# Kernel optimization log

Measured on AMD Instinct MI355X. Metric: run time of the kernel, lower is better.

## Reference

```python
import jax, jax.numpy as jnp
import numpy as np

DEPTH, DIM, HEADS, MLP_HID, POS_DIM, PROJ_DIM, NCLS, INP = 5, 128, 8, 256, 128, 128, 1000, 35
EPS = 1e-5

def _ln(x, g, b):
    m = x.mean(-1, keepdims=True)
    v = ((x - m) ** 2).mean(-1, keepdims=True)
    return (x - m) / jnp.sqrt(v + EPS) * g + b

def _gelu(x):
    return jax.nn.gelu(x, approximate=False)  # torch nn.GELU default (erf)

def setup_inputs() -> dict:
    key = jax.random.key(0)
    ks = iter(jax.random.split(key, 80))
    nxt = lambda: next(ks)
    B, N = 8, 1024
    w = lambda *s: (jax.random.normal(nxt(), s, jnp.float32) / np.sqrt(s[-2]).astype(np.float32))
    z = lambda *s: jnp.zeros(s, jnp.float32)
    o = lambda *s: jnp.ones(s, jnp.float32)
    node_feat = jax.random.normal(nxt(), (B, N, 3), jnp.float32)
    a = (jax.random.uniform(nxt(), (B, N, N)) < 0.01).astype(jnp.float32)
    adj = jnp.maximum(a, a.transpose(0, 2, 1))  # symmetric 0/1 adjacency
    lapl = jax.random.normal(nxt(), (B, N, 32), jnp.float32) * 0.1
    d = dict(
        node_feat=node_feat, adj=adj, lapl=lapl,
        cls_token=jax.random.normal(nxt(), (1, 1, DIM), jnp.float32),
        pe_w1=w(INP, 2 * INP), pe_b1=z(2 * INP),
        pe_w2=w(2 * INP, 2 * INP), pe_b2=z(2 * INP),
        pe_w3=w(2 * INP, 2 * INP), pe_b3=z(2 * INP),
        pe_lng=o(2 * INP), pe_lnb=z(2 * INP),
        pe_w4=w(2 * INP, POS_DIM), pe_b4=z(POS_DIM),
        blk_ln1_g=o(DEPTH, DIM), blk_ln1_b=z(DEPTH, DIM),
        blk_qkv_w=w(DEPTH, DIM, 3 * HEADS * DIM),
        blk_proj_w=w(DEPTH, HEADS * DIM, DIM), blk_proj_b=z(DEPTH, DIM),
        blk_gamma_w=jax.random.uniform(nxt(), (DEPTH, DIM, 2), jnp.float32) * 0.01,
        blk_gamma_b=z(DEPTH, 2),
        blk_ln2_g=o(DEPTH, DIM), blk_ln2_b=z(DEPTH, DIM),
        blk_mlp_w1=w(DEPTH, DIM, MLP_HID), blk_mlp_b1=z(DEPTH, MLP_HID),
        blk_mlp_w2=w(DEPTH, MLP_HID, DIM), blk_mlp_b2=z(DEPTH, DIM),
        head_lng=o(DIM), head_lnb=z(DIM), head_w=w(DIM, DIM), head_b=z(DIM),
        proj_w1=w(DIM, PROJ_DIM), proj_b1=z(PROJ_DIM),
        proj_w2=w(PROJ_DIM, PROJ_DIM), proj_b2=z(PROJ_DIM),
        proj_w3=w(PROJ_DIM, PROJ_DIM), proj_b3=z(PROJ_DIM),
        proj_lng=o(PROJ_DIM), proj_lnb=z(PROJ_DIM),
        proj_w4=w(PROJ_DIM, NCLS), proj_b4=z(NCLS),
    )
    return d

def reference(node_feat, adj, lapl, cls_token, pe_w1, pe_b1, pe_w2, pe_b2, pe_w3, pe_b3,
              pe_lng, pe_lnb, pe_w4, pe_b4, blk_ln1_g, blk_ln1_b, blk_qkv_w, blk_proj_w,
              blk_proj_b, blk_gamma_w, blk_gamma_b, blk_ln2_g, blk_ln2_b, blk_mlp_w1,
              blk_mlp_b1, blk_mlp_w2, blk_mlp_b2, head_lng, head_lnb, head_w, head_b,
              proj_w1, proj_b1, proj_w2, proj_b2, proj_w3, proj_b3, proj_lng, proj_lnb,
              proj_w4, proj_b4):
    B, N, _ = node_feat.shape
    M = N + 1
    # positional-encoding MLP on concatenated [node_feat | lapl] (inp_dim = 35)
    x = jnp.concatenate([node_feat, lapl], axis=2)
    x = _gelu(x @ pe_w1 + pe_b1)
    x = _gelu(x @ pe_w2 + pe_b2)
    x = _gelu(x @ pe_w3 + pe_b3)
    x = _ln(x, pe_lng, pe_lnb) @ pe_w4 + pe_b4  # [B,N,DIM]
    x = jnp.concatenate([jnp.broadcast_to(cls_token, (B, 1, DIM)), x], axis=1)  # [B,M,DIM]
    # adjacency with cls row/col, adj_cls[:,0,0] = 1
    adj_cls = jnp.zeros((B, M, M), x.dtype).at[:, 0, 0].set(1.0).at[:, 1:, 1:].set(adj)
    scale = DIM ** (-0.5)
    for i in range(DEPTH):
        h = _ln(x, blk_ln1_g[i], blk_ln1_b[i])
        qkv = (h @ blk_qkv_w[i]).reshape(B, M, 3, HEADS, DIM).transpose(2, 0, 3, 1, 4)
        q, k, v = qkv[0], qkv[1], qkv[2]  # each [B,H,M,D]
        attn = jnp.einsum('bhnd,bhmd->bhnm', q, k) * scale
        gamma = jnp.exp(h @ blk_gamma_w[i] + blk_gamma_b[i])  # [B,M,2], use_exp=True
        attn = gamma[:, None, :, 0:1] * attn + gamma[:, None, :, 1:2] * adj_cls[:, None]
        attn = jax.nn.softmax(attn, axis=-1)
        o = jnp.einsum('bhnm,bhmd->bhnd', attn, v).transpose(0, 2, 1, 3).reshape(B, M, HEADS * DIM)
        x = o @ blk_proj_w[i] + blk_proj_b[i] + h  # residual from normed input (as in source)
        h2 = _ln(x, blk_ln2_g[i], blk_ln2_b[i])
        x = _gelu(h2 @ blk_mlp_w1[i] + blk_mlp_b1[i]) @ blk_mlp_w2[i] + blk_mlp_b2[i] + h2
    c = x[:, 0]
    c = _ln(c, head_lng, head_lnb) @ head_w + head_b  # mlp_head
    p = _gelu(c @ proj_w1 + proj_b1)
    p = _gelu(p @ proj_w2 + proj_b2)
    p = _gelu(p @ proj_w3 + proj_b3)
    p = _ln(p, proj_lng, proj_lnb) @ proj_w4 + proj_b4
    return (c, p)
```

## Files before the change

### kernel.cpp

```cpp
#include <hip/hip_runtime.h>
#include <hip/hip_bf16.h>
#include <math.h>

#define NB 8
#define NSEQ 1024
#define M_ 1025
#define ROWS (NB * M_)
#define DIMC 128
#define NHEADS 8
#define QKV3 3072
#define PEROWS (NB * NSEQ)
#define ACS 1088

typedef __attribute__((ext_vector_type(8))) short bf16x8;
typedef __attribute__((ext_vector_type(4))) float f32x4;

__device__ __forceinline__ float gelu_f(float x) {
  return 0.5f * x * (1.f + erff(x * 0.70710678118654752440f));
}

__device__ __forceinline__ unsigned short f2bf(float f) {
  __hip_bfloat16 h = __float2bfloat16(f);
  return *reinterpret_cast<unsigned short*>(&h);
}

__device__ __forceinline__ float bf2f(unsigned short u) {
  union { unsigned int i; float f; } c;
  c.i = ((unsigned int)u) << 16;
  return c.f;
}

__device__ __forceinline__ void g2lds16(const void* g, void* l) {
  __builtin_amdgcn_global_load_lds(
      (__attribute__((address_space(1))) void*)(g),
      (__attribute__((address_space(3))) void*)(l), 16, 0, 0);
}

template<int K, int KP, int C, int SS, int DOGELU>
__device__ __forceinline__ void pe_stage(
    int tid, const float* __restrict__ W, const float* __restrict__ B,
    const float* src, float* dst, float (*wb)[128])
{
  for (int i = tid; i < K * C; i += 128) wb[i / C][i % C] = W[i];
  if (tid < C) {
#pragma unroll
    for (int k = K; k < KP; ++k) wb[k][tid] = 0.f;
  }
  __syncthreads();
  if (tid < C) {
    float acc[16];
#pragma unroll
    for (int r = 0; r < 16; ++r) acc[r] = B[tid];
#pragma unroll 1
    for (int k4 = 0; k4 < KP; k4 += 4) {
      const float w0 = wb[k4 + 0][tid];
      const float w1 = wb[k4 + 1][tid];
      const float w2 = wb[k4 + 2][tid];
      const float w3 = wb[k4 + 3][tid];
#pragma unroll
      for (int r = 0; r < 16; ++r) {
        const float4 av = *(const float4*)&src[r * SS + k4];
        acc[r] = fmaf(av.x, w0, acc[r]);
        acc[r] = fmaf(av.y, w1, acc[r]);
        acc[r] = fmaf(av.z, w2, acc[r]);
        acc[r] = fmaf(av.w, w3, acc[r]);
      }
    }
#pragma unroll
    for (int r = 0; r < 16; ++r) dst[r * 72 + tid] = DOGELU ? gelu_f(acc[r]) : acc[r];
  }
  __syncthreads();
}

__global__ __launch_bounds__(128) void pe_fused_k(
    const float* __restrict__ nf, const float* __restrict__ lp,
    const float* __restrict__ w1, const float* __restrict__ b1,
    const float* __restrict__ w2, const float* __restrict__ b2,
    const float* __restrict__ w3, const float* __restrict__ b3,
    const float* __restrict__ lng, const float* __restrict__ lnb,
    const float* __restrict__ w4, const float* __restrict__ b4,
    float* __restrict__ x)
{
  __shared__ float sIn[16][36];
  __shared__ float sX[16][72];
  __shared__ float sY[16][72];
  __shared__ float wb[72][128];
  const int tid = threadIdx.x;
  const int r0 = blockIdx.x * 16;

  for (int i = tid; i < 16 * 35; i += 128) {
    const int r = i / 35, c = i - r * 35;
    const int gr = r0 + r;
    sIn[r][c] = (c < 3) ? nf[(size_t)gr * 3 + c] : lp[(size_t)gr * 32 + (c - 3)];
  }
  if (tid < 16) {
    sIn[tid][35] = 0.f;
    sX[tid][70] = 0.f; sX[tid][71] = 0.f;
    sY[tid][70] = 0.f; sY[tid][71] = 0.f;
  }
  __syncthreads();

  pe_stage<35, 36, 70, 36, 1>(tid, w1, b1, &sIn[0][0], &sX[0][0], wb);
  pe_stage<70, 72, 70, 72, 1>(tid, w2, b2, &sX[0][0], &sY[0][0], wb);
  pe_stage<70, 72, 70, 72, 1>(tid, w3, b3, &sY[0][0], &sX[0][0], wb);

  if (tid < 16) {
    float m = 0.f;
    for (int d = 0; d < 70; ++d) m += sX[tid][d];
    m *= (1.f / 70.f);
    float v = 0.f;
    for (int d = 0; d < 70; ++d) { const float t = sX[tid][d] - m; v += t * t; }
    const float inv = rsqrtf(v * (1.f / 70.f) + 1e-5f);
    for (int d = 0; d < 70; ++d) sX[tid][d] = (sX[tid][d] - m) * inv * lng[d] + lnb[d];
  }
  __syncthreads();

  {
    for (int i = tid; i < 70 * 128; i += 128) wb[i >> 7][i & 127] = w4[i];
#pragma unroll
    for (int k = 70; k < 72; ++k) wb[k][tid] = 0.f;
    __syncthreads();
    float acc[16];
#pragma unroll
    for (int r = 0; r < 16; ++r) acc[r] = b4[tid];
#pragma unroll 1
    for (int k4 = 0; k4 < 72; k4 += 4) {
      const float w0 = wb[k4 + 0][tid];
      const float w1v = wb[k4 + 1][tid];
      const float w2v = wb[k4 + 2][tid];
      const float w3v = wb[k4 + 3][tid];
#pragma unroll
      for (int r = 0; r < 16; ++r) {
        const float4 av = *(const float4*)&sX[r][k4];
        acc[r] = fmaf(av.x, w0, acc[r]);
        acc[r] = fmaf(av.y, w1v, acc[r]);
        acc[r] = fmaf(av.z, w2v, acc[r]);
        acc[r] = fmaf(av.w, w3v, acc[r]);
      }
    }
#pragma unroll
    for (int r = 0; r < 16; ++r) {
      const int gr = r0 + r;
      x[(size_t)(gr + gr / 1024 + 1) * DIMC + tid] = acc[r];
    }
  }
}

template<int ACT, int OBF, int RES>
__global__ __launch_bounds__(256) void mgemm_k(
    const unsigned short* __restrict__ Xb, const unsigned short* __restrict__ Wt,
    const float* __restrict__ bias, const float* __restrict__ res,
    void* __restrict__ outp, int rows, int K, int N)
{
  __shared__ unsigned short sX[64][72];
  __shared__ unsigned short sW[64][72];
  const int tid = threadIdx.x;
  const int w = tid >> 6, lane = tid & 63;
  const int col = lane & 15, quad = lane >> 4;
  const int r0 = blockIdx.x * 64, n0 = blockIdx.y * 64;
  const int lr = tid >> 2, lc = tid & 3;
  const int xrow = min(r0 + lr, rows - 1);
  const unsigned short* xsrc = Xb + (size_t)xrow * K + lc * 8;
  const unsigned short* wsrc = Wt + (size_t)(n0 + lr) * K + lc * 8;

  f32x4 acc[4];
#pragma unroll
  for (int t = 0; t < 4; ++t) acc[t] = (f32x4){0.f, 0.f, 0.f, 0.f};

  for (int k0 = 0; k0 < K; k0 += 64) {
    __syncthreads();
    *(uint4*)&sX[lr][lc * 8]      = *(const uint4*)(xsrc + k0);
    *(uint4*)&sX[lr][lc * 8 + 32] = *(const uint4*)(xsrc + k0 + 32);
    *(uint4*)&sW[lr][lc * 8]      = *(const uint4*)(wsrc + k0);
    *(uint4*)&sW[lr][lc * 8 + 32] = *(const uint4*)(wsrc + k0 + 32);
    __syncthreads();
    const bf16x8 aX0 = *(const bf16x8*)&sX[w * 16 + col][quad * 8];
    const bf16x8 aX1 = *(const bf16x8*)&sX[w * 16 + col][32 + quad * 8];
#pragma unroll
    for (int t = 0; t < 4; ++t) {
      const bf16x8 bW0 = *(const bf16x8*)&sW[t * 16 + col][quad * 8];
      const bf16x8 bW1 = *(const bf16x8*)&sW[t * 16 + col][32 + quad * 8];
      acc[t] = __builtin_amdgcn_mfma_f32_16x16x32_bf16(aX0, bW0, acc[t], 0, 0, 0);
      acc[t] = __builtin_amdgcn_mfma_f32_16x16x32_bf16(aX1, bW1, acc[t], 0, 0, 0);
    }
  }
  const int gr_base = r0 + w * 16 + quad * 4;
#pragma unroll
  for (int t = 0; t < 4; ++t) {
    const int n = n0 + t * 16 + col;
    const float bv = bias ? bias[n] : 0.f;
#pragma unroll
    for (int r = 0; r < 4; ++r) {
      const int gr = gr_base + r;
      if (gr < rows) {
        float v = acc[t][r] + bv;
        if (ACT) v = gelu_f(v);
        if (RES) v += res[(size_t)gr * N + n];
        if (OBF) ((unsigned short*)outp)[(size_t)gr * N + n] = f2bf(v);
        else     ((float*)outp)[(size_t)gr * N + n] = v;
      }
    }
  }
}

template<int DOLN, int GAMMA, int WRITEX>
__global__ __launch_bounds__(256) void mgemm_ln_k(
    const unsigned short* __restrict__ Xb, const unsigned short* __restrict__ Wt,
    const float* __restrict__ bias, const float* __restrict__ res,
    const float* __restrict__ lng, const float* __restrict__ lnb,
    const float* __restrict__ gw, const float* __restrict__ gb,
    float* __restrict__ xout, float* __restrict__ h,
    unsigned short* __restrict__ hb, float* __restrict__ gamout,
    int rows, int K)
{
  __shared__ unsigned short sX[64][72];
  __shared__ unsigned short sW[128][72];
  const int tid = threadIdx.x;
  const int w = tid >> 6, lane = tid & 63;
  const int col = lane & 15, quad = lane >> 4;
  const int r0 = blockIdx.x * 64;

  f32x4 acc[8];
#pragma unroll
  for (int t = 0; t < 8; ++t) acc[t] = (f32x4){0.f, 0.f, 0.f, 0.f};

  for (int k0 = 0; k0 < K; k0 += 64) {
    __syncthreads();
#pragma unroll
    for (int l = 0; l < 2; ++l) {
      const int idx = l * 256 + tid;
      const int row = idx >> 3, c = idx & 7;
      const int xrow = min(r0 + row, rows - 1);
      *(uint4*)&sX[row][c * 8] = *(const uint4*)(Xb + (size_t)xrow * K + k0 + c * 8);
    }
#pragma unroll
    for (int l = 0; l < 4; ++l) {
      const int idx = l * 256 + tid;
      const int row = idx >> 3, c = idx & 7;
      *(uint4*)&sW[row][c * 8] = *(const uint4*)(Wt + (size_t)row * K + k0 + c * 8);
    }
    __syncthreads();
    const bf16x8 aX0 = *(const bf16x8*)&sX[w * 16 + col][quad * 8];
    const bf16x8 aX1 = *(const bf16x8*)&sX[w * 16 + col][32 + quad * 8];
#pragma unroll
    for (int t = 0; t < 8; ++t) {
      const bf16x8 bW0 = *(const bf16x8*)&sW[t * 16 + col][quad * 8];
      const bf16x8 bW1 = *(const bf16x8*)&sW[t * 16 + col][32 + quad * 8];
      acc[t] = __builtin_amdgcn_mfma_f32_16x16x32_bf16(aX0, bW0, acc[t], 0, 0, 0);
      acc[t] = __builtin_amdgcn_mfma_f32_16x16x32_bf16(aX1, bW1, acc[t], 0, 0, 0);
    }
  }

  const int gr_base = r0 + w * 16 + quad * 4;
  float bv[8];
#pragma unroll
  for (int t = 0; t < 8; ++t) bv[t] = bias[t * 16 + col];
  float val[8][4];
#pragma unroll
  for (int r = 0; r < 4; ++r) {
    const int grc = min(gr_base + r, rows - 1);
#pragma unroll
    for (int t = 0; t < 8; ++t)
      val[t][r] = acc[t][r] + bv[t] + res[(size_t)grc * DIMC + t * 16 + col];
  }
  if (WRITEX) {
#pragma unroll
    for (int r = 0; r < 4; ++r) {
      const int gr = gr_base + r;
      if (gr < rows) {
#pragma unroll
        for (int t = 0; t < 8; ++t)
          xout[(size_t)gr * DIMC + t * 16 + col] = val[t][r];
      }
    }
  }
  if (DOLN) {
    float lg[8], lb[8], gwa[8], gwb[8];
#pragma unroll
    for (int t = 0; t < 8; ++t) {
      lg[t] = lng[t * 16 + col];
      lb[t] = lnb[t * 16 + col];
      if (GAMMA) { gwa[t] = gw[2 * (t * 16 + col)]; gwb[t] = gw[2 * (t * 16 + col) + 1]; }
    }
#pragma unroll
    for (int r = 0; r < 4; ++r) {
      const int gr = gr_base + r;
      float s = 0.f;
#pragma unroll
      for (int t = 0; t < 8; ++t) s += val[t][r];
      s += __shfl_xor(s, 1); s += __shfl_xor(s, 2);
      s += __shfl_xor(s, 4); s += __shfl_xor(s, 8);
      const float mean = s * (1.f / 128.f);
      float vv = 0.f;
#pragma unroll
      for (int t = 0; t < 8; ++t) { const float d = val[t][r] - mean; vv += d * d; }
      vv += __shfl_xor(vv, 1); vv += __shfl_xor(vv, 2);
      vv += __shfl_xor(vv, 4); vv += __shfl_xor(vv, 8);
      const float inv = rsqrtf(vv * (1.f / 128.f) + 1e-5f);
      float a0 = 0.f, a1 = 0.f;
#pragma unroll
      for (int t = 0; t < 8; ++t) {
        const float o = (val[t][r] - mean) * inv * lg[t] + lb[t];
        if (gr < rows) {
          h[(size_t)gr * DIMC + t * 16 + col] = o;
          hb[(size_t)gr * DIMC + t * 16 + col] = f2bf(o);
        }
        if (GAMMA) { a0 = fmaf(o, gwa[t], a0); a1 = fmaf(o, gwb[t], a1); }
      }
      if (GAMMA) {
        a0 += __shfl_xor(a0, 1); a0 += __shfl_xor(a0, 2);
        a0 += __shfl_xor(a0, 4); a0 += __shfl_xor(a0, 8);
        a1 += __shfl_xor(a1, 1); a1 += __shfl_xor(a1, 2);
        a1 += __shfl_xor(a1, 4); a1 += __shfl_xor(a1, 8);
        if (col == 0 && gr < rows) {
          gamout[(size_t)gr * 2 + 0] = expf(a0 + gb[0]);
          gamout[(size_t)gr * 2 + 1] = expf(a1 + gb[1]);
        }
      }
    }
  }
}

template<int OBF, int VT>
__global__ __launch_bounds__(256) void mgemm128_k(
    const unsigned short* __restrict__ Xb, const unsigned short* __restrict__ Wt,
    const float* __restrict__ bias, void* __restrict__ outp,
    unsigned short* __restrict__ vtp, int rows, int K, int N)
{
  __shared__ unsigned short sX[128][72];
  __shared__ unsigned short sW[128][72];
  const int tid = threadIdx.x;
  const int w = tid >> 6, lane = tid & 63;
  const int col = lane & 15, quad = lane >> 4;
  const int wr = w >> 1, wc = w & 1;
  const int r0 = blockIdx.x * 128, n0 = blockIdx.y * 128;

  f32x4 acc[4][4];
#pragma unroll
  for (int i = 0; i < 4; ++i)
#pragma unroll
    for (int j = 0; j < 4; ++j) acc[i][j] = (f32x4){0.f, 0.f, 0.f, 0.f};

  for (int k0 = 0; k0 < K; k0 += 64) {
    __syncthreads();
#pragma unroll
    for (int l = 0; l < 4; ++l) {
      const int idx = l * 256 + tid;
      const int row = idx >> 3, c = idx & 7;
      const int xrow = min(r0 + row, rows - 1);
      *(uint4*)&sX[row][c * 8] = *(const uint4*)(Xb + (size_t)xrow * K + k0 + c * 8);
      *(uint4*)&sW[row][c * 8] = *(const uint4*)(Wt + (size_t)(n0 + row) * K + k0 + c * 8);
    }
    __syncthreads();
    bf16x8 aX[4][2];
#pragma unroll
    for (int i = 0; i < 4; ++i) {
      aX[i][0] = *(const bf16x8*)&sX[wr * 64 + i * 16 + col][quad * 8];
      aX[i][1] = *(const bf16x8*)&sX[wr * 64 + i * 16 + col][32 + quad * 8];
    }
#pragma unroll
    for (int j = 0; j < 4; ++j) {
      const bf16x8 b0 = *(const bf16x8*)&sW[wc * 64 + j * 16 + col][quad * 8];
      const bf16x8 b1 = *(const bf16x8*)&sW[wc * 64 + j * 16 + col][32 + quad * 8];
#pragma unroll
      for (int i = 0; i < 4; ++i) {
        acc[i][j] = __builtin_amdgcn_mfma_f32_16x16x32_bf16(aX[i][0], b0, acc[i][j], 0, 0, 0);
        acc[i][j] = __builtin_amdgcn_mfma_f32_16x16x32_bf16(aX[i][1], b1, acc[i][j], 0, 0, 0);
      }
    }
  }
  const bool dovt = VT && (n0 >= 2048);
#pragma unroll
  for (int i = 0; i < 4; ++i) {
    const int gr_base = r0 + wr * 64 + i * 16 + quad * 4;
    int bb[4], mm[4];
    if (dovt) {
#pragma unroll
      for (int r = 0; r < 4; ++r) {
        const int gr = gr_base + r;
        bb[r] = gr / 1025;
        mm[r] = gr - bb[r] * 1025;
      }
    }
#pragma unroll
    for (int j = 0; j < 4; ++j) {
      const int n = n0 + wc * 64 + j * 16 + col;
      const float bv = bias ? bias[n] : 0.f;
      const int hh = (n - 2048) >> 7;
      const int d  = (n - 2048) & 127;
#pragma unroll
      for (int r = 0; r < 4; ++r) {
        const int gr = gr_base + r;
        if (gr < rows) {
          const float v = acc[i][j][r] + bv;
          const unsigned short bf = f2bf(v);
          if (OBF) ((unsigned short*)outp)[(size_t)gr * N + n] = bf;
          else     ((float*)outp)[(size_t)gr * N + n] = v;
          if (dovt) vtp[(((size_t)(bb[r] * NHEADS + hh) * DIMC + d) * ACS) + mm[r]] = bf;
        }
      }
    }
  }
}

__global__ __launch_bounds__(256) void ln_rows_k(
    const float* __restrict__ in, float* __restrict__ out,
    unsigned short* __restrict__ outb,
    const float* __restrict__ g, const float* __restrict__ b,
    const float* __restrict__ gw, const float* __restrict__ gb,
    float* __restrict__ gamout, int rows, int D)
{
  const int wv = (blockIdx.x * blockDim.x + threadIdx.x) >> 6;
  const int lane = threadIdx.x & 63;
  if (wv >= rows) return;
  const float* r = in + (size_t)wv * D;
  float s = 0.f;
  for (int d = lane; d < D; d += 64) s += r[d];
  for (int off = 32; off; off >>= 1) s += __shfl_down(s, off);
  const float mean = __shfl(s, 0) / (float)D;
  float v = 0.f;
  for (int d = lane; d < D; d += 64) { float t = r[d] - mean; v += t * t; }
  for (int off = 32; off; off >>= 1) v += __shfl_down(v, off);
  const float inv = rsqrtf(__shfl(v, 0) / (float)D + 1e-5f);
  float* orow = out + (size_t)wv * D;
  float a0 = 0.f, a1 = 0.f;
  for (int d = lane; d < D; d += 64) {
    const float o = (r[d] - mean) * inv * g[d] + b[d];
    orow[d] = o;
    if (outb) outb[(size_t)wv * D + d] = f2bf(o);
    if (gw) { a0 = fmaf(o, gw[2 * d], a0); a1 = fmaf(o, gw[2 * d + 1], a1); }
  }
  if (gw) {
    for (int off = 32; off; off >>= 1) { a0 += __shfl_down(a0, off); a1 += __shfl_down(a1, off); }
    if (lane == 0) {
      gamout[(size_t)wv * 2 + 0] = expf(a0 + gb[0]);
      gamout[(size_t)wv * 2 + 1] = expf(a1 + gb[1]);
    }
  }
}

__global__ __launch_bounds__(256) void adjp_k(const float* __restrict__ adj,
                                              unsigned long long* __restrict__ adjp)
{
  const int n = blockIdx.x;
  const int b = blockIdx.y;
  const int wv = threadIdx.x >> 6, lane = threadIdx.x & 63;
  for (int w = wv; w < 17; w += 4) {
    const int m = w * 64 + lane;
    float av = 0.f;
    if (n == 0) av = (m == 0) ? 1.f : 0.f;
    else if (m >= 1 && m <= NSEQ) av = adj[((size_t)b * NSEQ + (n - 1)) * NSEQ + (m - 1)];
    const unsigned long long mask = __ballot(av != 0.f);
    if (lane == 0) adjp[((size_t)b * M_ + n) * 17 + w] = mask;
  }
}

__global__ void wtrans_k(const float* __restrict__ W, unsigned short* __restrict__ Wt,
                         int K, int N)
{
  __shared__ float t[32][33];
  const int k0 = blockIdx.x * 32, n0 = blockIdx.y * 32;
  const float* Wd = W + (size_t)blockIdx.z * K * N;
  unsigned short* Wtd = Wt + (size_t)blockIdx.z * K * N;
  for (int i = threadIdx.y; i < 32; i += 8)
    t[i][threadIdx.x] = Wd[(size_t)(k0 + i) * N + n0 + threadIdx.x];
  __syncthreads();
  for (int i = threadIdx.y; i < 32; i += 8)
    Wtd[(size_t)(n0 + i) * K + k0 + threadIdx.x] = f2bf(t[threadIdx.x][i]);
}

__global__ __launch_bounds__(512) void attn_mfma_k(
    const unsigned short* __restrict__ qkv, const float* __restrict__ gamma,
    const unsigned long long* __restrict__ adjp, const unsigned short* __restrict__ vt,
    unsigned short* __restrict__ o)
{
  __shared__ unsigned short sK[2][64][128];
  __shared__ unsigned short sVt[2][128][64];
  __shared__ unsigned short sP[256][64];

  const int hh = blockIdx.x, qt = blockIdx.y, b = blockIdx.z;
  const int tid = threadIdx.x;
  const int w = tid >> 6;
  const int lane = tid & 63;
  const int col = lane & 15;
  const int quad = lane >> 4;
  const int qbase = qt * 256 + w * 32;
  const float scale = 0.088388347648318447f;

  bf16x8 aQ[2][4];
#pragma unroll
  for (int rg = 0; rg < 2; ++rg) {
    const int qrow = qbase + rg * 16 + col;
    const unsigned short* qp = qkv + ((size_t)(b * M_ + qrow)) * QKV3 + hh * DIMC + quad * 8;
#pragma unroll
    for (int c = 0; c < 4; ++c) aQ[rg][c] = *(const bf16x8*)(qp + c * 32);
  }
  float g0[2][4], g1[2][4];
  int adjo[2][4];
#pragma unroll
  for (int rg = 0; rg < 2; ++rg)
#pragma unroll
    for (int r = 0; r < 4; ++r) {
      const int nc = qbase + rg * 16 + quad * 4 + r;
      g0[rg][r] = gamma[(size_t)(b * M_ + nc) * 2 + 0] * scale;
      g1[rg][r] = gamma[(size_t)(b * M_ + nc) * 2 + 1];
      adjo[rg][r] = (b * M_ + nc) * 17;
    }

  float l_i[2][4] = {{0.f, 0.f, 0.f, 0.f}, {0.f, 0.f, 0.f, 0.f}};
  f32x4 Oacc[2][8];
#pragma unroll
  for (int rg = 0; rg < 2; ++rg)
#pragma unroll
    for (int t = 0; t < 8; ++t) Oacc[rg][t] = (f32x4){0.f, 0.f, 0.f, 0.f};

  const size_t vtbase = ((size_t)(b * NHEADS + hh)) * DIMC * ACS;

  auto stageK = [&](int buf, int kt_) {
#pragma unroll
    for (int l = 0; l < 2; ++l) {
      const int m = l * 32 + w * 4 + (lane >> 4);
      const int gm = min(kt_ * 64 + m, 1024);
      const unsigned short* src = qkv + ((size_t)(b * M_ + gm)) * QKV3 + 1024
                                  + hh * DIMC + (((lane & 15) ^ (m & 7)) * 8);
      g2lds16(src, &sK[buf][l * 32 + w * 4][0]);
    }
  };
  auto stageV = [&](int buf, int kt_) {
#pragma unroll
    for (int l = 0; l < 2; ++l) {
      const int d = l * 64 + w * 8 + (lane >> 3);
      const unsigned short* src = vt + vtbase + (size_t)d * ACS + kt_ * 64
                                  + (((lane & 7) ^ (d & 7)) * 8);
      g2lds16(src, &sVt[buf][l * 64 + w * 8][0]);
    }
  };

  stageK(0, 0);
  stageV(0, 0);

  int cur = 0;
  for (int kt = 0; kt < 17; ++kt) {
    const int m0 = kt * 64;
    asm volatile("s_waitcnt vmcnt(0)" ::: "memory");
    __builtin_amdgcn_s_barrier();
    __builtin_amdgcn_sched_barrier(0);

    const bool more = (kt < 16);
    if (more) {
      stageK(cur ^ 1, kt + 1);
      stageV(cur ^ 1, kt + 1);
    }

    unsigned long long mk[2][4];
#pragma unroll
    for (int rg = 0; rg < 2; ++rg)
#pragma unroll
      for (int r = 0; r < 4; ++r) mk[rg][r] = adjp[adjo[rg][r] + kt];

    f32x4 Sacc[2][4];
#pragma unroll
    for (int rg = 0; rg < 2; ++rg)
#pragma unroll
      for (int t = 0; t < 4; ++t) Sacc[rg][t] = (f32x4){0.f, 0.f, 0.f, 0.f};
    __builtin_amdgcn_s_setprio(1);
#pragma unroll
    for (int t = 0; t < 4; ++t) {
#pragma unroll
      for (int c = 0; c < 4; ++c) {
        const bf16x8 bK = *(const bf16x8*)&sK[cur][t * 16 + col][((c * 4 + quad) ^ (col & 7)) * 8];
        Sacc[0][t] = __builtin_amdgcn_mfma_f32_16x16x32_bf16(aQ[0][c], bK, Sacc[0][t], 0, 0, 0);
        Sacc[1][t] = __builtin_amdgcn_mfma_f32_16x16x32_bf16(aQ[1][c], bK, Sacc[1][t], 0, 0, 0);
      }
    }
    __builtin_amdgcn_s_setprio(0);

#pragma unroll
    for (int t = 0; t < 4; ++t) {
      const int m = m0 + t * 16 + col;
      const bool mv = (m < M_);
      const int chb = t * 2 + (col >> 3);
      const int sh = t * 16 + col;
#pragma unroll
      for (int rg = 0; rg < 2; ++rg)
#pragma unroll
        for (int r = 0; r < 4; ++r) {
          const float bias = ((mk[rg][r] >> sh) & 1ull) ? g1[rg][r] : 0.f;
          const float s = fmaf(g0[rg][r], Sacc[rg][t][r], bias);
          const float pv = mv ? __expf(s) : 0.f;
          l_i[rg][r] += pv;
          const int ql = w * 32 + rg * 16 + quad * 4 + r;
          sP[ql][((chb ^ (ql & 7)) * 8) + (col & 7)] = f2bf(pv);
        }
    }

    __builtin_amdgcn_s_setprio(1);
#pragma unroll
    for (int ch = 0; ch < 2; ++ch) {
      const int pr = w * 32 + col;
      const bf16x8 aP0 = *(const bf16x8*)&sP[pr][((ch * 4 + quad) ^ (col & 7)) * 8];
      const bf16x8 aP1 = *(const bf16x8*)&sP[pr + 16][((ch * 4 + quad) ^ (col & 7)) * 8];
#pragma unroll
      for (int t = 0; t < 8; ++t) {
        const bf16x8 bV = *(const bf16x8*)&sVt[cur][t * 16 + col][((ch * 4 + quad) ^ (col & 7)) * 8];
        Oacc[0][t] = __builtin_amdgcn_mfma_f32_16x16x32_bf16(aP0, bV, Oacc[0][t], 0, 0, 0);
        Oacc[1][t] = __builtin_amdgcn_mfma_f32_16x16x32_bf16(aP1, bV, Oacc[1][t], 0, 0, 0);
      }
    }
    __builtin_amdgcn_s_setprio(0);
    cur ^= 1;
  }

#pragma unroll
  for (int rg = 0; rg < 2; ++rg)
#pragma unroll
    for (int r = 0; r < 4; ++r) {
      float s = l_i[rg][r];
      s += __shfl_xor(s, 1);
      s += __shfl_xor(s, 2);
      s += __shfl_xor(s, 4);
      s += __shfl_xor(s, 8);
      const int n = qbase + rg * 16 + quad * 4 + r;
      const float invl = 1.f / s;
      unsigned short* orow = o + ((size_t)(b * M_ + n)) * (NHEADS * DIMC) + hh * DIMC + col;
#pragma unroll
      for (int t = 0; t < 8; ++t) orow[t * 16] = f2bf(Oacc[rg][t][r] * invl);
    }
}

__global__ __launch_bounds__(256) void cls_attn_k(
    const unsigned short* __restrict__ qkv, const float* __restrict__ gamma,
    const unsigned long long* __restrict__ adjp, const unsigned short* __restrict__ vt,
    unsigned short* __restrict__ o)
{
  __shared__ float qf[DIMC];
  __shared__ float pbuf[1056];
  __shared__ float lred[4];
  __shared__ float oshare[DIMC];
  const int hh = blockIdx.x & 7, b = blockIdx.x >> 3;
  const int tid = threadIdx.x;
  const size_t rowbase = (size_t)b * M_ + 1024;

  if (tid < DIMC) qf[tid] = bf2f(qkv[rowbase * QKV3 + hh * DIMC + tid]);
  __syncthreads();
  const float g0 = gamma[rowbase * 2 + 0] * 0.088388347648318447f;
  const float g1 = gamma[rowbase * 2 + 1];

  float lpart = 0.f;
  for (int m = tid; m < M_; m += 256) {
    const unsigned short* kp = qkv + ((size_t)(b * M_ + m)) * QKV3 + 1024 + hh * DIMC;
    float s = 0.f;
#pragma unroll
    for (int d0 = 0; d0 < DIMC; d0 += 8) {
      const bf16x8 kv = *(const bf16x8*)(kp + d0);
#pragma unroll
      for (int j = 0; j < 8; ++j)
        s = fmaf(bf2f((unsigned short)kv[j]), qf[d0 + j], s);
    }
    const unsigned long long mkv = adjp[rowbase * 17 + (m >> 6)];
    const float bias = ((mkv >> (m & 63)) & 1ull) ? g1 : 0.f;
    const float p = __expf(fmaf(g0, s, bias));
    pbuf[m] = p;
    lpart += p;
  }
  for (int off = 32; off; off >>= 1) lpart += __shfl_down(lpart, off);
  if ((tid & 63) == 0) lred[tid >> 6] = lpart;
  __syncthreads();
  const float linv = 1.f / (lred[0] + lred[1] + lred[2] + lred[3]);

  const int d = tid & 127, half = tid >> 7;
  const unsigned short* vrow = vt + ((size_t)(b * NHEADS + hh)) * DIMC * ACS + (size_t)d * ACS;
  float acc = 0.f;
  const int mstart = half * 512;
  const int mend = half ? 1024 : 512;
  for (int m0 = mstart; m0 < mend; m0 += 8) {
    const bf16x8 vv = *(const bf16x8*)(vrow + m0);
#pragma unroll
    for (int j = 0; j < 8; ++j)
      acc = fmaf(bf2f((unsigned short)vv[j]), pbuf[m0 + j], acc);
  }
  if (half) acc = fmaf(bf2f(vrow[1024]), pbuf[1024], acc);
  if (half == 0) oshare[d] = acc;
  __syncthreads();
  if (half == 1) {
    const float val = (oshare[d] + acc) * linv;
    o[rowbase * (NHEADS * DIMC) + hh * DIMC + d] = f2bf(val);
  }
}

template<int DOLN, int ACT>
__global__ __launch_bounds__(256) void hstage_k(
    const float* __restrict__ in, int in_stride,
    const float* __restrict__ lng, const float* __restrict__ lnb,
    const float* __restrict__ W, const float* __restrict__ bias,
    float* __restrict__ out)
{
  __shared__ float xn[8][128];
  __shared__ float red[128];
  const int tid = threadIdx.x;
  for (int i = tid; i < 1024; i += 256) {
    const int r = i >> 7, d = i & 127;
    xn[r][d] = in[(size_t)r * in_stride + d];
  }
  __syncthreads();
  if (DOLN) {
    const int wv = tid >> 6, lane = tid & 63;
    const int row = wv * 2 + (lane >> 5);
    const int l32 = lane & 31;
    float s = 0.f;
    for (int d = l32; d < 128; d += 32) s += xn[row][d];
    for (int off = 16; off; off >>= 1) s += __shfl_xor(s, off);
    const float mean = s * (1.f / 128.f);
    float v = 0.f;
    for (int d = l32; d < 128; d += 32) { const float t = xn[row][d] - mean; v += t * t; }
    for (int off = 16; off; off >>= 1) v += __shfl_xor(v, off);
    const float inv = rsqrtf(v * (1.f / 128.f) + 1e-5f);
    for (int d = l32; d < 128; d += 32)
      xn[row][d] = (xn[row][d] - mean) * inv * lng[d] + lnb[d];
    __syncthreads();
  }
  const int col = blockIdx.x * 16 + (tid & 15);
  const int row = (tid >> 4) & 7;
  const int ks = tid >> 7;
  float acc = 0.f;
  const int kb = ks * 64;
  for (int k = kb; k < kb + 64; ++k)
    acc = fmaf(xn[row][k], W[k * 128 + col], acc);
  if (ks) red[tid - 128] = acc;
  __syncthreads();
  if (!ks) {
    float v = acc + red[tid] + bias[col];
    if (ACT) v = gelu_f(v);
    out[row * 128 + col] = v;
  }
}

__global__ __launch_bounds__(256) void hfinal_k(
    const float* __restrict__ in,
    const float* __restrict__ plg, const float* __restrict__ plb,
    const float* __restrict__ W, const float* __restrict__ bias,
    float* __restrict__ out_p)
{
  __shared__ float xn[128];
  const int r = blockIdx.x & 7, cc = blockIdx.x >> 3;
  const int tid = threadIdx.x;
  const int lane = tid & 63;
  const float a = in[r * 128 + lane];
  const float b = in[r * 128 + 64 + lane];
  float s = a + b;
  for (int off = 32; off; off >>= 1) s += __shfl_xor(s, off);
  const float mean = s * (1.f / 128.f);
  const float t0 = a - mean, t1 = b - mean;
  float v = t0 * t0 + t1 * t1;
  for (int off = 32; off; off >>= 1) v += __shfl_xor(v, off);
  const float inv = rsqrtf(v * (1.f / 128.f) + 1e-5f);
  if (tid < 128) xn[tid] = (in[r * 128 + tid] - mean) * inv * plg[tid] + plb[tid];
  __syncthreads();
  const int col = cc * 250 + tid;
  if (tid < 250) {
    float acc = bias[col];
    for (int k = 0; k < 128; ++k)
      acc = fmaf(xn[k], W[(size_t)k * 1000 + col], acc);
    out_p[r * 1000 + col] = acc;
  }
}

__global__ void fill_cls_k(const float* __restrict__ cls, float* __restrict__ x)
{
  x[(size_t)blockIdx.x * M_ * DIMC + threadIdx.x] = cls[threadIdx.x];
}

extern "C" void kernel_launch(void* const* d_in, const int* in_sizes, int n_in,
                              void* d_out, int out_size, void* d_ws, size_t ws_size,
                              hipStream_t stream)
{
  (void)in_sizes; (void)n_in; (void)out_size; (void)ws_size;
  const float* node_feat = (const float*)d_in[0];
  const float* adj       = (const float*)d_in[1];
  const float* lapl      = (const float*)d_in[2];
  const float* cls_token = (const float*)d_in[3];
  const float* pe_w1 = (const float*)d_in[4];
  const float* pe_b1 = (const float*)d_in[5];
  const float* pe_w2 = (const float*)d_in[6];
  const float* pe_b2 = (const float*)d_in[7];
  const float* pe_w3 = (const float*)d_in[8];
  const float* pe_b3 = (const float*)d_in[9];
  const float* pe_lng = (const float*)d_in[10];
  const float* pe_lnb = (const float*)d_in[11];
  const float* pe_w4 = (const float*)d_in[12];
  const float* pe_b4 = (const float*)d_in[13];
  const float* blk_ln1_g = (const float*)d_in[14];
  const float* blk_ln1_b = (const float*)d_in[15];
  const float* blk_qkv_w = (const float*)d_in[16];
  const float* blk_proj_w = (const float*)d_in[17];
  const float* blk_proj_b = (const float*)d_in[18];
  const float* blk_gamma_w = (const float*)d_in[19];
  const float* blk_gamma_b = (const float*)d_in[20];
  const float* blk_ln2_g = (const float*)d_in[21];
  const float* blk_ln2_b = (const float*)d_in[22];
  const float* blk_mlp_w1 = (const float*)d_in[23];
  const float* blk_mlp_b1 = (const float*)d_in[24];
  const float* blk_mlp_w2 = (const float*)d_in[25];
  const float* blk_mlp_b2 = (const float*)d_in[26];
  const float* head_lng = (const float*)d_in[27];
  const float* head_lnb = (const float*)d_in[28];
  const float* head_w = (const float*)d_in[29];
  const float* head_b = (const float*)d_in[30];
  const float* proj_w1 = (const float*)d_in[31];
  const float* proj_b1 = (const float*)d_in[32];
  const float* proj_w2 = (const float*)d_in[33];
  const float* proj_b2 = (const float*)d_in[34];
  const float* proj_w3 = (const float*)d_in[35];
  const float* proj_b3 = (const float*)d_in[36];
  const float* proj_lng = (const float*)d_in[37];
  const float* proj_lnb = (const float*)d_in[38];
  const float* proj_w4 = (const float*)d_in[39];
  const float* proj_b4 = (const float*)d_in[40];

  float* ws   = (float*)d_ws;
  float* x    = ws;
  float* h    = x + 1049600;
  float* gam  = h + 1049600;
  float* obuf = gam + 16400;
  unsigned short* obufb = (unsigned short*)obuf;
  unsigned short* hidb  = (unsigned short*)(obuf + 4198400);
  float* sm  = obuf + 5248000;
  unsigned short* hb   = (unsigned short*)(sm + 8192);
  unsigned short* qkv  = hb + 1049600;
  unsigned long long* adjp = (unsigned long long*)(qkv + 25190400);
  unsigned short* vt   = (unsigned short*)(adjp + 139400 + 88);
  unsigned short* qkvWt = vt + 8912896;
  unsigned short* projWt = qkvWt + 5 * 393216;
  unsigned short* mlp1Wt = projWt + 5 * 131072;
  unsigned short* mlp2Wt = mlp1Wt + 5 * 32768;

  float* out_c = (float*)d_out;
  float* out_p = out_c + NB * DIMC;
  float* p1 = sm;
  float* p2 = sm + 1024;

  adjp_k<<<dim3(M_, NB), 256, 0, stream>>>(adj, adjp);
  wtrans_k<<<dim3(4, 96, 5), dim3(32, 8), 0, stream>>>(blk_qkv_w, qkvWt, 128, 3072);
  wtrans_k<<<dim3(32, 4, 5), dim3(32, 8), 0, stream>>>(blk_proj_w, projWt, 1024, 128);
  wtrans_k<<<dim3(4, 8, 5), dim3(32, 8), 0, stream>>>(blk_mlp_w1, mlp1Wt, 128, 256);
  wtrans_k<<<dim3(8, 4, 5), dim3(32, 8), 0, stream>>>(blk_mlp_w2, mlp2Wt, 256, 128);

  pe_fused_k<<<512, 128, 0, stream>>>(node_feat, lapl, pe_w1, pe_b1, pe_w2, pe_b2,
                                      pe_w3, pe_b3, pe_lng, pe_lnb, pe_w4, pe_b4, x);
  fill_cls_k<<<NB, DIMC, 0, stream>>>(cls_token, x);

  const int lnGrid = (ROWS * 64 + 255) / 256;
  ln_rows_k<<<lnGrid, 256, 0, stream>>>(x, h, hb, blk_ln1_g, blk_ln1_b,
                                        blk_gamma_w, blk_gamma_b, gam, ROWS, DIMC);

  for (int i = 0; i < 5; ++i) {
    const float* pb   = blk_proj_b + i * DIMC;
    const float* ln2g = blk_ln2_g + i * DIMC;
    const float* ln2b = blk_ln2_b + i * DIMC;
    const float* mb1  = blk_mlp_b1 + i * 256;
    const float* mb2  = blk_mlp_b2 + i * DIMC;
    const unsigned short* qw = qkvWt + (size_t)i * 393216;
    const unsigned short* pw = projWt + (size_t)i * 131072;
    const unsigned short* m1w = mlp1Wt + (size_t)i * 32768;
    const unsigned short* m2w = mlp2Wt + (size_t)i * 32768;

    mgemm128_k<1, 1><<<dim3(65, 24), 256, 0, stream>>>(hb, qw, nullptr, qkv, vt, ROWS, 128, 3072);
    attn_mfma_k<<<dim3(NHEADS, 4, NB), 512, 0, stream>>>(qkv, gam, adjp, vt, obufb);
    cls_attn_k<<<64, 256, 0, stream>>>(qkv, gam, adjp, vt, obufb);

    mgemm_ln_k<1, 0, 0><<<129, 256, 0, stream>>>(
        obufb, pw, pb, h, ln2g, ln2b, nullptr, nullptr,
        nullptr, h, hb, nullptr, ROWS, 1024);

    mgemm_k<1, 1, 0><<<dim3(129, 4), 256, 0, stream>>>(hb, m1w, mb1, nullptr, hidb, ROWS, 128, 256);

    if (i < 4) {
      const float* nln1g = blk_ln1_g + (i + 1) * DIMC;
      const float* nln1b = blk_ln1_b + (i + 1) * DIMC;
      const float* ngw   = blk_gamma_w + (size_t)(i + 1) * DIMC * 2;
      const float* ngb   = blk_gamma_b + (i + 1) * 2;
      mgemm_ln_k<1, 1, 0><<<129, 256, 0, stream>>>(
          hidb, m2w, mb2, h, nln1g, nln1b, ngw, ngb,
          nullptr, h, hb, gam, ROWS, 256);
    } else {
      mgemm_ln_k<0, 0, 1><<<129, 256, 0, stream>>>(
          hidb, m2w, mb2, h, nullptr, nullptr, nullptr, nullptr,
          x, nullptr, nullptr, nullptr, ROWS, 256);
    }
  }

  hstage_k<1, 0><<<8, 256, 0, stream>>>(x, M_ * DIMC, head_lng, head_lnb,
                                        head_w, head_b, out_c);
  hstage_k<0, 1><<<8, 256, 0, stream>>>(out_c, 128, nullptr, nullptr,
                                        proj_w1, proj_b1, p1);
  hstage_k<0, 1><<<8, 256, 0, stream>>>(p1, 128, nullptr, nullptr,
                                        proj_w2, proj_b2, p2);
  hstage_k<0, 1><<<8, 256, 0, stream>>>(p2, 128, nullptr, nullptr,
                                        proj_w3, proj_b3, p1);
  hfinal_k<<<32, 256, 0, stream>>>(p1, proj_lng, proj_lnb, proj_w4, proj_b4, out_p);
}
```

Baseline: 1.374 ms.

## Halve row tile in fused GEMM+LayerNorm kernel and split columns across waves

The fused GEMM+LayerNorm kernel now processes 32 rows per block instead of 64. Its four waves form a 2x2 grid of row groups by column halves, and the launch count roughly doubles from 129 blocks. Because each row is now split between two waves, the LayerNorm statistics and the gamma projection are combined through shared memory. Variance is computed in a single pass as E[x^2]-mean^2. The aim is better GPU occupancy for the K=1024 projection and K=256 MLP GEMMs. The cost is more weight-tile reloads per row, extra barriers, and slightly weaker numerics for the variance.

```diff
diff --git a/kernel.cpp b/kernel.cpp
--- a/kernel.cpp
+++ b/kernel.cpp
@@ -213,23 +213,26 @@
     unsigned short* __restrict__ hb, float* __restrict__ gamout,
     int rows, int K)
 {
-  __shared__ unsigned short sX[64][72];
+  __shared__ unsigned short sX[32][72];
   __shared__ unsigned short sW[128][72];
+  __shared__ float redS[2][32];
+  __shared__ float redQ[2][32];
+  __shared__ float redA0[2][32];
+  __shared__ float redA1[2][32];
   const int tid = threadIdx.x;
   const int w = tid >> 6, lane = tid & 63;
   const int col = lane & 15, quad = lane >> 4;
-  const int r0 = blockIdx.x * 64;
-
-  f32x4 acc[8];
-#pragma unroll
-  for (int t = 0; t < 8; ++t) acc[t] = (f32x4){0.f, 0.f, 0.f, 0.f};
+  const int rg = w >> 1, ch = w & 1;
+  const int r0 = blockIdx.x * 32;
+
+  f32x4 acc[4];
+#pragma unroll
+  for (int t = 0; t < 4; ++t) acc[t] = (f32x4){0.f, 0.f, 0.f, 0.f};
 
   for (int k0 = 0; k0 < K; k0 += 64) {
     __syncthreads();
-#pragma unroll
-    for (int l = 0; l < 2; ++l) {
-      const int idx = l * 256 + tid;
-      const int row = idx >> 3, c = idx & 7;
+    {
+      const int row = tid >> 3, c = tid & 7;
       const int xrow = min(r0 + row, rows - 1);
       *(uint4*)&sX[row][c * 8] = *(const uint4*)(Xb + (size_t)xrow * K + k0 + c * 8);
     }
@@ -240,28 +243,27 @@
       *(uint4*)&sW[row][c * 8] = *(const uint4*)(Wt + (size_t)row * K + k0 + c * 8);
     }
     __syncthreads();
-    const bf16x8 aX0 = *(const bf16x8*)&sX[w * 16 + col][quad * 8];
-    const bf16x8 aX1 = *(const bf16x8*)&sX[w * 16 + col][32 + quad * 8];
-#pragma unroll
-    for (int t = 0; t < 8; ++t) {
-      const bf16x8 bW0 = *(const bf16x8*)&sW[t * 16 + col][quad * 8];
-      const bf16x8 bW1 = *(const bf16x8*)&sW[t * 16 + col][32 + quad * 8];
+    const bf16x8 aX0 = *(const bf16x8*)&sX[rg * 16 + col][quad * 8];
+    const bf16x8 aX1 = *(const bf16x8*)&sX[rg * 16 + col][32 + quad * 8];
+#pragma unroll
+    for (int t = 0; t < 4; ++t) {
+      const bf16x8 bW0 = *(const bf16x8*)&sW[ch * 64 + t * 16 + col][quad * 8];
+      const bf16x8 bW1 = *(const bf16x8*)&sW[ch * 64 + t * 16 + col][32 + quad * 8];
       acc[t] = __builtin_amdgcn_mfma_f32_16x16x32_bf16(aX0, bW0, acc[t], 0, 0, 0);
       acc[t] = __builtin_amdgcn_mfma_f32_16x16x32_bf16(aX1, bW1, acc[t], 0, 0, 0);
     }
   }
 
-  const int gr_base = r0 + w * 16 + quad * 4;
-  float bv[8];
-#pragma unroll
-  for (int t = 0; t < 8; ++t) bv[t] = bias[t * 16 + col];
-  float val[8][4];
+  const int gr_base = r0 + rg * 16 + quad * 4;
+  float val[4][4];
 #pragma unroll
   for (int r = 0; r < 4; ++r) {
     const int grc = min(gr_base + r, rows - 1);
 #pragma unroll
-    for (int t = 0; t < 8; ++t)
-      val[t][r] = acc[t][r] + bv[t] + res[(size_t)grc * DIMC + t * 16 + col];
+    for (int t = 0; t < 4; ++t) {
+      const int n = ch * 64 + t * 16 + col;
+      val[t][r] = acc[t][r] + bias[n] + res[(size_t)grc * DIMC + n];
+    }
   }
   if (WRITEX) {
 #pragma unroll
@@ -269,41 +271,53 @@
       const int gr = gr_base + r;
       if (gr < rows) {
 #pragma unroll
-        for (int t = 0; t < 8; ++t)
-          xout[(size_t)gr * DIMC + t * 16 + col] = val[t][r];
+        for (int t = 0; t < 4; ++t)
+          xout[(size_t)gr * DIMC + ch * 64 + t * 16 + col] = val[t][r];
       }
     }
   }
   if (DOLN) {
-    float lg[8], lb[8], gwa[8], gwb[8];
-#pragma unroll
-    for (int t = 0; t < 8; ++t) {
-      lg[t] = lng[t * 16 + col];
-      lb[t] = lnb[t * 16 + col];
-      if (GAMMA) { gwa[t] = gw[2 * (t * 16 + col)]; gwb[t] = gw[2 * (t * 16 + col) + 1]; }
-    }
 #pragma unroll
     for (int r = 0; r < 4; ++r) {
-      const int gr = gr_base + r;
-      float s = 0.f;
-#pragma unroll
-      for (int t = 0; t < 8; ++t) s += val[t][r];
+      float s = 0.f, q = 0.f;
+#pragma unroll
+      for (int t = 0; t < 4; ++t) { s += val[t][r]; q = fmaf(val[t][r], val[t][r], q); }
       s += __shfl_xor(s, 1); s += __shfl_xor(s, 2);
       s += __shfl_xor(s, 4); s += __shfl_xor(s, 8);
-      const float mean = s * (1.f / 128.f);
-      float vv = 0.f;
-#pragma unroll
-      for (int t = 0; t < 8; ++t) { const float d = val[t][r] - mean; vv += d * d; }
-      vv += __shfl_xor(vv, 1); vv += __shfl_xor(vv, 2);
-      vv += __shfl_xor(vv, 4); vv += __shfl_xor(vv, 8);
-      const float inv = rsqrtf(vv * (1.f / 128.f) + 1e-5f);
+      q += __shfl_xor(q, 1); q += __shfl_xor(q, 2);
+      q += __shfl_xor(q, 4); q += __shfl_xor(q, 8);
+      if (col == 0) {
+        const int rl = rg * 16 + quad * 4 + r;
+        redS[ch][rl] = s;
+        redQ[ch][rl] = q;
+      }
+    }
+    __syncthreads();
+    float lg[4], lb[4], gwa[4], gwb[4];
+#pragma unroll
+    for (int t = 0; t < 4; ++t) {
+      const int n = ch * 64 + t * 16 + col;
+      lg[t] = lng[n];
+      lb[t] = lnb[n];
+      if (GAMMA) { gwa[t] = gw[2 * n]; gwb[t] = gw[2 * n + 1]; }
+    }
+#pragma unroll
+    for (int r = 0; r < 4; ++r) {
+      const int rl = rg * 16 + quad * 4 + r;
+      const int gr = gr_base + r;
+      const float S = redS[0][rl] + redS[1][rl];
+      const float Q = redQ[0][rl] + redQ[1][rl];
+      const float mean = S * (1.f / 128.f);
+      const float var = Q * (1.f / 128.f) - mean * mean;
+      const float inv = rsqrtf(var + 1e-5f);
       float a0 = 0.f, a1 = 0.f;
 #pragma unroll
-      for (int t = 0; t < 8; ++t) {
+      for (int t = 0; t < 4; ++t) {
         const float o = (val[t][r] - mean) * inv * lg[t] + lb[t];
         if (gr < rows) {
-          h[(size_t)gr * DIMC + t * 16 + col] = o;
-          hb[(size_t)gr * DIMC + t * 16 + col] = f2bf(o);
+          const int n = ch * 64 + t * 16 + col;
+          h[(size_t)gr * DIMC + n] = o;
+          hb[(size_t)gr * DIMC + n] = f2bf(o);
         }
         if (GAMMA) { a0 = fmaf(o, gwa[t], a0); a1 = fmaf(o, gwb[t], a1); }
       }
@@ -312,9 +326,18 @@
         a0 += __shfl_xor(a0, 4); a0 += __shfl_xor(a0, 8);
         a1 += __shfl_xor(a1, 1); a1 += __shfl_xor(a1, 2);
         a1 += __shfl_xor(a1, 4); a1 += __shfl_xor(a1, 8);
-        if (col == 0 && gr < rows) {
-          gamout[(size_t)gr * 2 + 0] = expf(a0 + gb[0]);
-          gamout[(size_t)gr * 2 + 1] = expf(a1 + gb[1]);
+        if (col == 0) { redA0[ch][rl] = a0; redA1[ch][rl] = a1; }
+      }
+    }
+    if (GAMMA) {
+      __syncthreads();
+#pragma unroll
+      for (int r = 0; r < 4; ++r) {
+        const int rl = rg * 16 + quad * 4 + r;
+        const int gr = gr_base + r;
+        if (ch == 0 && col == 0 && gr < rows) {
+          gamout[(size_t)gr * 2 + 0] = expf(redA0[0][rl] + redA0[1][rl] + gb[0]);
+          gamout[(size_t)gr * 2 + 1] = expf(redA1[0][rl] + redA1[1][rl] + gb[1]);
         }
       }
     }
@@ -853,6 +876,7 @@
   ln_rows_k<<<lnGrid, 256, 0, stream>>>(x, h, hb, blk_ln1_g, blk_ln1_b,
                                         blk_gamma_w, blk_gamma_b, gam, ROWS, DIMC);
 
+  const int fGrid = (ROWS + 31) / 32;
   for (int i = 0; i < 5; ++i) {
     const float* pb   = blk_proj_b + i * DIMC;
     const float* ln2g = blk_ln2_g + i * DIMC;
@@ -868,7 +892,7 @@
     attn_mfma_k<<<dim3(NHEADS, 4, NB), 512, 0, stream>>>(qkv, gam, adjp, vt, obufb);
     cls_attn_k<<<64, 256, 0, stream>>>(qkv, gam, adjp, vt, obufb);
 
-    mgemm_ln_k<1, 0, 0><<<129, 256, 0, stream>>>(
+    mgemm_ln_k<1, 0, 0><<<fGrid, 256, 0, stream>>>(
         obufb, pw, pb, h, ln2g, ln2b, nullptr, nullptr,
         nullptr, h, hb, nullptr, ROWS, 1024);
 
@@ -879,11 +903,11 @@
       const float* nln1b = blk_ln1_b + (i + 1) * DIMC;
       const float* ngw   = blk_gamma_w + (size_t)(i + 1) * DIMC * 2;
       const float* ngb   = blk_gamma_b + (i + 1) * 2;
-      mgemm_ln_k<1, 1, 0><<<129, 256, 0, stream>>>(
+      mgemm_ln_k<1, 1, 0><<<fGrid, 256, 0, stream>>>(
           hidb, m2w, mb2, h, nln1g, nln1b, ngw, ngb,
           nullptr, h, hb, gam, ROWS, 256);
     } else {
-      mgemm_ln_k<0, 0, 1><<<129, 256, 0, stream>>>(
+      mgemm_ln_k<0, 0, 1><<<fGrid, 256, 0, stream>>>(
           hidb, m2w, mb2, h, nullptr, nullptr, nullptr, nullptr,
           x, nullptr, nullptr, nullptr, ROWS, 256);
     }
```

Result: faster. 1.326 ms (-3.4%).
